# Kernel optimization log

Measured on AMD Instinct MI355X. Metric: run time of the kernel, lower is better.

## Reference

```python
import jax, jax.numpy as jnp
import numpy as np

B = 16384   # batch (agents x parallel envs)
IN = 12     # input_dim
H = 64      # hidden_dim -> 2H = 128
OUT = 25    # output_dim (forced by x[:,0:5]..x[:,20:25] slicing)


def setup_inputs() -> dict:
    key = jax.random.key(0)
    ks = jax.random.split(key, 24)
    n = lambda k, s: jax.random.normal(k, s, dtype=jnp.float32)
    s = 0.1  # scale params to keep SiLU/softmax in a sane range
    return {
        "x": n(ks[0], (B, IN)),
        "na": 4,
        # mlp_in: Linear(IN, 2H) + SiLU
        "W_in": n(ks[1], (2 * H, IN)) * s, "b_in": n(ks[2], (2 * H,)) * s,
        # first attention (2H)
        "Aq4": n(ks[3], (2 * H, 2 * H)) * s, "Bq4": n(ks[4], (2 * H,)) * s,
        "Ak4": n(ks[5], (2 * H, 2 * H)) * s, "Bk4": n(ks[6], (2 * H,)) * s,
        "Av4": n(ks[7], (2 * H, 2 * H)) * s, "Bv4": n(ks[8], (2 * H,)) * s,
        # mlp_hidden_4: Linear(2H, H) + SiLU
        "W_h": n(ks[9], (H, 2 * H)) * s, "b_h": n(ks[10], (H,)) * s,
        # second attention (H)
        "Aq7": n(ks[11], (H, H)) * s, "Bq7": n(ks[12], (H,)) * s,
        "Ak7": n(ks[13], (H, H)) * s, "Bk7": n(ks[14], (H,)) * s,
        "Av7": n(ks[15], (H, H)) * s, "Bv7": n(ks[16], (H,)) * s,
        # mlp_out: Linear(H, OUT) + SiLU
        "W_out": n(ks[17], (OUT, H)) * s, "b_out": n(ks[18], (OUT,)) * s,
    }


def _attn(h, Aq, Bq, Ak, Bk, Av, Bv):
    # h: [B, D]; torch does bmm(A, x^T)+B with x of shape [B,1,D] -> seq-len-1
    # attention, i.e. scores are an outer product q k^T of shape [B, D, D].
    q = jax.nn.silu(h @ Aq.T + Bq)                      # [B, D]
    k = jax.nn.silu(h @ Ak.T + Bk)                      # [B, D]
    v = jax.nn.silu(h @ Av.T + Bv)                      # [B, D]
    a = jax.nn.softmax(q[:, :, None] * k[:, None, :], axis=2)  # [B, D, D]
    return jax.nn.silu(jnp.einsum("bij,bj->bi", a, v))  # [B, D]


def reference(x, na, W_in, b_in, Aq4, Bq4, Ak4, Bk4, Av4, Bv4,
              W_h, b_h, Aq7, Bq7, Ak7, Bk7, Av7, Bv7, W_out, b_out):
    h = jax.nn.silu(x @ W_in.T + b_in)                  # [B, 2H]
    h = _attn(h, Aq4, Bq4, Ak4, Bk4, Av4, Bv4)          # [B, 2H]
    h = jax.nn.silu(h @ W_h.T + b_h)                    # [B, H]
    h = _attn(h, Aq7, Bq7, Ak7, Bk7, Av7, Bv7)          # [B, H]
    y = jax.nn.silu(h @ W_out.T + b_out)                # [B, 25]

    # block-diagonal quadratic-form assembly (l=2, kron with ones(1,2))
    M11 = jnp.sum(y[:, 0:5] ** 2, axis=1)               # [B]
    M12 = jnp.sum(y[:, 5:10] ** 2, axis=1)
    M21 = jnp.sum(y[:, 10:15] ** 2, axis=1)
    M22 = jnp.sum(y[:, 15:20] ** 2, axis=1)
    Mpp = jnp.sum(y[:, 20:25] ** 2, axis=1)             # [B]
    q = y[:, :4]                                        # [B, 4] = [q0,q1,q2,q3]
    # M = [[diag(M11), diag(M12)],[diag(M21), diag(M22)]] (each 2x2 diag)
    quad = (M11 * (q[:, 0] ** 2 + q[:, 1] ** 2)
            + (M12 + M21) * (q[:, 0] * q[:, 2] + q[:, 1] * q[:, 3])
            + M22 * (q[:, 2] ** 2 + q[:, 3] ** 2))
    return (quad + Mpp)[:, None]                        # [B, 1]
```

## Files before the change

### kernel.cpp

```cpp
#include <hip/hip_runtime.h>

#define RPW 4
#define WAVES 4
#define RPB (RPW * WAVES)
#define NM 14

using short8 = __attribute__((ext_vector_type(8))) short;
using f32x4  = __attribute__((ext_vector_type(4))) float;

#define LOG2E 1.4426950408889634f

static __device__ __forceinline__ float ex2(float x) { return __builtin_amdgcn_exp2f(x); }
static __device__ __forceinline__ float rcpf_(float x) { return __builtin_amdgcn_rcpf(x); }
static __device__ __forceinline__ float silu_(float x) {
    return x * rcpf_(1.0f + ex2(-x * LOG2E));
}
static __device__ __forceinline__ unsigned short bfhi(float x) {
    return (unsigned short)(__float_as_uint(x) >> 16);
}
static __device__ __forceinline__ unsigned short bfrn(float x) {
    unsigned u = __float_as_uint(x);
    return (unsigned short)((u + 0x7fffu + ((u >> 16) & 1u)) >> 16);
}
static __device__ __forceinline__ float bf2f(unsigned short h) {
    return __uint_as_float(((unsigned)h) << 16);
}

__constant__ float c_invfact[15] = {
    1.f, 1.f, 0.5f, 1.f/6, 1.f/24, 1.f/120, 1.f/720, 1.f/5040, 1.f/40320,
    1.f/362880, 1.f/3628800, 1.f/39916800, 1.f/479001600,
    1.f/6227020800.f, 1.f/87178291200.f};

template <int O, int I>
__device__ __forceinline__ void tr(const float* __restrict__ s, float* __restrict__ d,
                                   int t0, int stride) {
    for (int idx = t0; idx < O * I; idx += stride) {
        int o = idx / I, in = idx - o * I;
        d[in * O + o] = s[idx];
    }
}
template <int N>
__device__ __forceinline__ void cvt(const float* __restrict__ s,
                                    unsigned short* __restrict__ hi,
                                    unsigned short* __restrict__ lo,
                                    int t0, int stride) {
    for (int i = t0; i < N; i += stride) {
        float a = s[i];
        unsigned short h = bfhi(a);
        float r = a - bf2f(h);
        hi[i] = h;
        lo[i] = bfhi(r);
    }
}

__global__ void tweights(const float* __restrict__ s0, const float* __restrict__ s1,
                         const float* __restrict__ s2, const float* __restrict__ s3,
                         const float* __restrict__ s4, const float* __restrict__ s5,
                         const float* __restrict__ s6, const float* __restrict__ s7,
                         const float* __restrict__ s8, float* __restrict__ ws) {
    const int stride = gridDim.x * blockDim.x;
    const int t0 = blockIdx.x * blockDim.x + threadIdx.x;
    tr<128, 12>(s0, ws + 0, t0, stride);
    unsigned short* u4 = (unsigned short*)(ws + 1536);
    cvt<128 * 128>(s1, u4 + 0,     u4 + 16384, t0, stride);
    cvt<128 * 128>(s2, u4 + 32768, u4 + 49152, t0, stride);
    cvt<128 * 128>(s3, u4 + 65536, u4 + 81920, t0, stride);
    unsigned short* wh = (unsigned short*)(ws + 50688);
    cvt<64 * 128>(s4, wh + 0, wh + 8192, t0, stride);
    unsigned short* u7 = (unsigned short*)(ws + 58880);
    cvt<64 * 64>(s5, u7 + 0,     u7 + 4096,  t0, stride);
    cvt<64 * 64>(s6, u7 + 8192,  u7 + 12288, t0, stride);
    cvt<64 * 64>(s7, u7 + 16384, u7 + 20480, t0, stride);
    tr<25, 64>(s8, ws + 71168, t0, stride);
}

__global__ __launch_bounds__(256, 4) void fused_net(
    const float* __restrict__ x, const float* __restrict__ ws,
    const float* __restrict__ b_in,
    const float* __restrict__ Bq4, const float* __restrict__ Bk4, const float* __restrict__ Bv4,
    const float* __restrict__ b_h,
    const float* __restrict__ Bq7, const float* __restrict__ Bk7, const float* __restrict__ Bv7,
    const float* __restrict__ b_out,
    float* __restrict__ out) {
    __shared__ __align__(16) unsigned short hAhi[16][136], hAlo[16][136];
    __shared__ __align__(16) unsigned short h2hi[16][80],  h2lo[16][80];
    __shared__ __align__(16) float sQ[16][132];
    __shared__ __align__(16) unsigned short sKVb[16][132][2];
    __shared__ __align__(16) float h3T[WAVES][64][RPW];
    __shared__ __align__(16) float sXT[WAVES][12][RPW];
    __shared__ __align__(16) float sY[WAVES][RPW][26];

    const int tid = threadIdx.x;
    const int w = tid >> 6;
    const int l = tid & 63;
    const int row0 = blockIdx.x * RPB + w * RPW;
    const int m16 = l & 15, quad = l >> 4;
    const int g = l & 15, r = l >> 4;
    const int R = w * RPW + r;

    const float* WinT  = ws + 0;
    const float* WoutT = ws + 71168;

    if (l < 12 * RPW) {
        float v = x[row0 * 12 + l];
        int rr = l / 12, in = l - rr * 12;
        sXT[w][in][rr] = v;
    }

    {
        float2 bb = *(const float2*)&b_in[2 * l];
        float a0[RPW], a1[RPW];
        #pragma unroll
        for (int rr = 0; rr < RPW; rr++) { a0[rr] = bb.x; a1[rr] = bb.y; }
        #pragma unroll
        for (int in = 0; in < 12; in++) {
            float2 wv = *(const float2*)&WinT[in * 128 + 2 * l];
            float4 xr = *(const float4*)&sXT[w][in][0];
            a0[0] = fmaf(xr.x, wv.x, a0[0]); a1[0] = fmaf(xr.x, wv.y, a1[0]);
            a0[1] = fmaf(xr.y, wv.x, a0[1]); a1[1] = fmaf(xr.y, wv.y, a1[1]);
            a0[2] = fmaf(xr.z, wv.x, a0[2]); a1[2] = fmaf(xr.z, wv.y, a1[2]);
            a0[3] = fmaf(xr.w, wv.x, a0[3]); a1[3] = fmaf(xr.w, wv.y, a1[3]);
        }
        #pragma unroll
        for (int rr = 0; rr < RPW; rr++) {
            float h0 = silu_(a0[rr]), h1 = silu_(a1[rr]);
            unsigned short h0h = bfhi(h0), h1h = bfhi(h1);
            float r0 = h0 - bf2f(h0h), r1 = h1 - bf2f(h1h);
            *(unsigned*)&hAhi[w * 4 + rr][2 * l] = (unsigned)h0h | ((unsigned)h1h << 16);
            *(unsigned*)&hAlo[w * 4 + rr][2 * l] = (unsigned)bfhi(r0) | ((unsigned)bfhi(r1) << 16);
        }
    }
    __syncthreads();

    {
        short8 Ah[4], Al[4];
        #pragma unroll
        for (int kt = 0; kt < 4; kt++) {
            Ah[kt] = *(const short8*)&hAhi[m16][kt * 32 + quad * 8];
            Al[kt] = *(const short8*)&hAlo[m16][kt * 32 + quad * 8];
        }
        const unsigned short* u4 = (const unsigned short*)(ws + 1536);
        #pragma unroll
        for (int t = 0; t < 6; t++) {
            const int nt = w * 6 + t;
            const int mat = nt >> 3;
            const int n = (nt & 7) * 16 + m16;
            const float* bp = (mat == 0) ? Bq4 : (mat == 1) ? Bk4 : Bv4;
            float b = bp[n];
            f32x4 acc = {b, b, b, b};
            const unsigned short* Bh = u4 + mat * 32768 + n * 128;
            const unsigned short* Bl = Bh + 16384;
            #pragma unroll
            for (int kt = 0; kt < 4; kt++) {
                short8 bh = *(const short8*)&Bh[kt * 32 + quad * 8];
                short8 bl = *(const short8*)&Bl[kt * 32 + quad * 8];
                acc = __builtin_amdgcn_mfma_f32_16x16x32_bf16(Ah[kt], bh, acc, 0, 0, 0);
                acc = __builtin_amdgcn_mfma_f32_16x16x32_bf16(Ah[kt], bl, acc, 0, 0, 0);
                acc = __builtin_amdgcn_mfma_f32_16x16x32_bf16(Al[kt], bh, acc, 0, 0, 0);
            }
            #pragma unroll
            for (int reg = 0; reg < 4; reg++) {
                int row = quad * 4 + reg;
                float val = silu_(acc[reg]);
                if (mat == 0)      sQ[row][n] = val;
                else if (mat == 1) sKVb[row][n][0] = bfrn(val);
                else               sKVb[row][n][1] = bfrn(val);
            }
        }
    }
    __syncthreads();

    {
        float dmom[NM];
        float nmom[NM + 1];
        #pragma unroll
        for (int m = 0; m < NM; m++) dmom[m] = 0.f;
        #pragma unroll
        for (int m = 0; m <= NM; m++) nmom[m] = 0.f;
        uint4 u0 = *(const uint4*)&sKVb[R][g * 8][0];
        uint4 u1 = *(const uint4*)&sKVb[R][g * 8 + 4][0];
        unsigned us[8] = {u0.x, u0.y, u0.z, u0.w, u1.x, u1.y, u1.z, u1.w};
        #pragma unroll
        for (int jj = 0; jj < 8; jj++) {
            unsigned u = us[jj];
            float kf = __uint_as_float(u << 16);
            float vf = __uint_as_float(u & 0xffff0000u);
            nmom[0] += vf;
            float p = kf;
            dmom[0] += p; nmom[1] = fmaf(vf, p, nmom[1]);
            #pragma unroll
            for (int m = 1; m < NM; m++) {
                p *= kf;
                dmom[m] += p;
                nmom[m + 1] = fmaf(vf, p, nmom[m + 1]);
            }
        }
        #pragma unroll
        for (int m = 0; m < NM; m++) {
            float v = dmom[m];
            v += __shfl_xor(v, 1); v += __shfl_xor(v, 2);
            v += __shfl_xor(v, 4); v += __shfl_xor(v, 8);
            dmom[m] = v;
        }
        #pragma unroll
        for (int m = 0; m <= NM; m++) {
            float v = nmom[m];
            v += __shfl_xor(v, 1); v += __shfl_xor(v, 2);
            v += __shfl_xor(v, 4); v += __shfl_xor(v, 8);
            nmom[m] = v;
        }
        float cd[NM + 1], cn[NM + 1];
        cd[0] = 128.f; cn[0] = nmom[0];
        #pragma unroll
        for (int m = 1; m <= NM; m++) {
            cd[m] = dmom[m - 1] * c_invfact[m];
            cn[m] = nmom[m] * c_invfact[m];
        }
        float4 qa = *(const float4*)&sQ[R][g * 8];
        float4 qb = *(const float4*)&sQ[R][g * 8 + 4];
        float qs[8] = {qa.x, qa.y, qa.z, qa.w, qb.x, qb.y, qb.z, qb.w};
        unsigned hiw[4], low[4];
        #pragma unroll
        for (int i = 0; i < 8; i++) {
            float t = qs[i];
            float d = cd[NM], nn = cn[NM];
            #pragma unroll
            for (int m = NM - 1; m >= 0; m--) {
                d = fmaf(d, t, cd[m]);
                nn = fmaf(nn, t, cn[m]);
            }
            float o = silu_(nn * rcpf_(d));
            unsigned short oh = bfhi(o);
            unsigned short olo = bfhi(o - bf2f(oh));
            if (i & 1) { hiw[i >> 1] |= ((unsigned)oh) << 16; low[i >> 1] |= ((unsigned)olo) << 16; }
            else       { hiw[i >> 1] = oh; low[i >> 1] = olo; }
        }
        *(uint4*)&hAhi[R][g * 8] = make_uint4(hiw[0], hiw[1], hiw[2], hiw[3]);
        *(uint4*)&hAlo[R][g * 8] = make_uint4(low[0], low[1], low[2], low[3]);
    }
    __syncthreads();

    {
        short8 Ah[4], Al[4];
        #pragma unroll
        for (int kt = 0; kt < 4; kt++) {
            Ah[kt] = *(const short8*)&hAhi[m16][kt * 32 + quad * 8];
            Al[kt] = *(const short8*)&hAlo[m16][kt * 32 + quad * 8];
        }
        const unsigned short* whh = (const unsigned short*)(ws + 50688);
        const unsigned short* whl = whh + 8192;
        const int n = w * 16 + m16;
        float b = b_h[n];
        f32x4 acc = {b, b, b, b};
        #pragma unroll
        for (int kt = 0; kt < 4; kt++) {
            short8 bh = *(const short8*)&whh[n * 128 + kt * 32 + quad * 8];
            short8 bl = *(const short8*)&whl[n * 128 + kt * 32 + quad * 8];
            acc = __builtin_amdgcn_mfma_f32_16x16x32_bf16(Ah[kt], bh, acc, 0, 0, 0);
            acc = __builtin_amdgcn_mfma_f32_16x16x32_bf16(Ah[kt], bl, acc, 0, 0, 0);
            acc = __builtin_amdgcn_mfma_f32_16x16x32_bf16(Al[kt], bh, acc, 0, 0, 0);
        }
        #pragma unroll
        for (int reg = 0; reg < 4; reg++) {
            int row = quad * 4 + reg;
            float hv = silu_(acc[reg]);
            unsigned short hh = bfhi(hv);
            h2hi[row][n] = hh;
            h2lo[row][n] = bfhi(hv - bf2f(hh));
        }
    }
    __syncthreads();

    {
        short8 Ah[2], Al[2];
        #pragma unroll
        for (int kt = 0; kt < 2; kt++) {
            Ah[kt] = *(const short8*)&h2hi[m16][kt * 32 + quad * 8];
            Al[kt] = *(const short8*)&h2lo[m16][kt * 32 + quad * 8];
        }
        const unsigned short* u7 = (const unsigned short*)(ws + 58880);
        #pragma unroll
        for (int t = 0; t < 3; t++) {
            const int nt = w * 3 + t;
            const int mat = nt >> 2;
            const int n = (nt & 3) * 16 + m16;
            const float* bp = (mat == 0) ? Bq7 : (mat == 1) ? Bk7 : Bv7;
            float b = bp[n];
            f32x4 acc = {b, b, b, b};
            const unsigned short* Bh = u7 + mat * 8192 + n * 64;
            const unsigned short* Bl = Bh + 4096;
            #pragma unroll
            for (int kt = 0; kt < 2; kt++) {
                short8 bh = *(const short8*)&Bh[kt * 32 + quad * 8];
                short8 bl = *(const short8*)&Bl[kt * 32 + quad * 8];
                acc = __builtin_amdgcn_mfma_f32_16x16x32_bf16(Ah[kt], bh, acc, 0, 0, 0);
                acc = __builtin_amdgcn_mfma_f32_16x16x32_bf16(Ah[kt], bl, acc, 0, 0, 0);
                acc = __builtin_amdgcn_mfma_f32_16x16x32_bf16(Al[kt], bh, acc, 0, 0, 0);
            }
            #pragma unroll
            for (int reg = 0; reg < 4; reg++) {
                int row = quad * 4 + reg;
                float val = silu_(acc[reg]);
                if (mat == 0)      sQ[row][n] = val;
                else if (mat == 1) sKVb[row][n][0] = bfrn(val);
                else               sKVb[row][n][1] = bfrn(val);
            }
        }
    }
    __syncthreads();

    {
        float dmom[NM];
        float nmom[NM + 1];
        #pragma unroll
        for (int m = 0; m < NM; m++) dmom[m] = 0.f;
        #pragma unroll
        for (int m = 0; m <= NM; m++) nmom[m] = 0.f;
        uint4 u0 = *(const uint4*)&sKVb[R][g * 4][0];
        unsigned us[4] = {u0.x, u0.y, u0.z, u0.w};
        #pragma unroll
        for (int jj = 0; jj < 4; jj++) {
            unsigned u = us[jj];
            float kf = __uint_as_float(u << 16);
            float vf = __uint_as_float(u & 0xffff0000u);
            nmom[0] += vf;
            float p = kf;
            dmom[0] += p; nmom[1] = fmaf(vf, p, nmom[1]);
            #pragma unroll
            for (int m = 1; m < NM; m++) {
                p *= kf;
                dmom[m] += p;
                nmom[m + 1] = fmaf(vf, p, nmom[m + 1]);
            }
        }
        #pragma unroll
        for (int m = 0; m < NM; m++) {
            float v = dmom[m];
            v += __shfl_xor(v, 1); v += __shfl_xor(v, 2);
            v += __shfl_xor(v, 4); v += __shfl_xor(v, 8);
            dmom[m] = v;
        }
        #pragma unroll
        for (int m = 0; m <= NM; m++) {
            float v = nmom[m];
            v += __shfl_xor(v, 1); v += __shfl_xor(v, 2);
            v += __shfl_xor(v, 4); v += __shfl_xor(v, 8);
            nmom[m] = v;
        }
        float cd[NM + 1], cn[NM + 1];
        cd[0] = 64.f; cn[0] = nmom[0];
        #pragma unroll
        for (int m = 1; m <= NM; m++) {
            cd[m] = dmom[m - 1] * c_invfact[m];
            cn[m] = nmom[m] * c_invfact[m];
        }
        float4 qa = *(const float4*)&sQ[R][g * 4];
        float qs[4] = {qa.x, qa.y, qa.z, qa.w};
        #pragma unroll
        for (int i = 0; i < 4; i++) {
            float t = qs[i];
            float d = cd[NM], nn = cn[NM];
            #pragma unroll
            for (int m = NM - 1; m >= 0; m--) {
                d = fmaf(d, t, cd[m]);
                nn = fmaf(nn, t, cn[m]);
            }
            h3T[w][g * 4 + i][r] = silu_(nn * rcpf_(d));
        }
    }

    {
        const int o = l & 31;
        const int half = l >> 5;
        const int oc = (o < 25) ? o : 0;
        float y[RPW];
        float bb = (half == 0) ? b_out[oc] : 0.f;
        #pragma unroll
        for (int rr = 0; rr < RPW; rr++) y[rr] = bb;
        const int in0 = half * 32;
        #pragma unroll 4
        for (int i = 0; i < 32; i++) {
            int in = in0 + i;
            float wv = WoutT[in * 25 + oc];
            float4 xr = *(const float4*)&h3T[w][in][0];
            y[0] = fmaf(xr.x, wv, y[0]);
            y[1] = fmaf(xr.y, wv, y[1]);
            y[2] = fmaf(xr.z, wv, y[2]);
            y[3] = fmaf(xr.w, wv, y[3]);
        }
        #pragma unroll
        for (int rr = 0; rr < RPW; rr++) {
            float full = y[rr] + __shfl_xor(y[rr], 32, 64);
            if (l < 25) sY[w][rr][l] = silu_(full);
        }
    }

    if (l < RPW) {
        const int rr = l;
        float y[25];
        #pragma unroll
        for (int c = 0; c < 25; c++) y[c] = sY[w][rr][c];
        float M11 = 0.f, M12 = 0.f, M21 = 0.f, M22 = 0.f, Mpp = 0.f;
        #pragma unroll
        for (int c = 0; c < 5; c++) {
            M11 = fmaf(y[c], y[c], M11);
            M12 = fmaf(y[5 + c], y[5 + c], M12);
            M21 = fmaf(y[10 + c], y[10 + c], M21);
            M22 = fmaf(y[15 + c], y[15 + c], M22);
            Mpp = fmaf(y[20 + c], y[20 + c], Mpp);
        }
        float quad = M11 * (y[0] * y[0] + y[1] * y[1])
                   + (M12 + M21) * (y[0] * y[2] + y[1] * y[3])
                   + M22 * (y[2] * y[2] + y[3] * y[3]);
        out[row0 + rr] = quad + Mpp;
    }
}

extern "C" void kernel_launch(void* const* d_in, const int* in_sizes, int n_in,
                              void* d_out, int out_size, void* d_ws, size_t ws_size,
                              hipStream_t stream) {
    const float* x    = (const float*)d_in[0];
    const float* W_in = (const float*)d_in[2];
    const float* b_in = (const float*)d_in[3];
    const float* Aq4  = (const float*)d_in[4];
    const float* Bq4  = (const float*)d_in[5];
    const float* Ak4  = (const float*)d_in[6];
    const float* Bk4  = (const float*)d_in[7];
    const float* Av4  = (const float*)d_in[8];
    const float* Bv4  = (const float*)d_in[9];
    const float* W_h  = (const float*)d_in[10];
    const float* b_h  = (const float*)d_in[11];
    const float* Aq7  = (const float*)d_in[12];
    const float* Bq7  = (const float*)d_in[13];
    const float* Ak7  = (const float*)d_in[14];
    const float* Bk7  = (const float*)d_in[15];
    const float* Av7  = (const float*)d_in[16];
    const float* Bv7  = (const float*)d_in[17];
    const float* Wout = (const float*)d_in[18];
    const float* bout = (const float*)d_in[19];
    float* ws = (float*)d_ws;

    tweights<<<128, 256, 0, stream>>>(W_in, Aq4, Ak4, Av4, W_h, Aq7, Ak7, Av7, Wout, ws);

    const int B = in_sizes[0] / 12;
    const int grid = B / RPB;
    fused_net<<<grid, 256, 0, stream>>>(x, ws, b_in, Bq4, Bk4, Bv4,
                                        b_h, Bq7, Bk7, Bv7, bout, (float*)d_out);
}
```

Before: 137.9 us.

## Truncate softmax moment series and split MFMA accumulator chains

Cuts the Taylor-moment expansion used for the outer-product softmax from 14 to 12 terms, removing per-element multiply-adds in the attention stages. The MFMA chains in the three projection GEMMs are split into two independent accumulators that are summed at the end, so dependent MFMA latency can overlap. The weight-preprocessing launch also doubles its grid. Fewer series terms lower accuracy for larger score magnitudes, so results may drift.

```diff
diff --git a/kernel.cpp b/kernel.cpp
--- a/kernel.cpp
+++ b/kernel.cpp
@@ -3,7 +3,7 @@
 #define RPW 4
 #define WAVES 4
 #define RPB (RPW * WAVES)
-#define NM 14
+#define NM 12
 
 using short8 = __attribute__((ext_vector_type(8))) short;
 using f32x4  = __attribute__((ext_vector_type(4))) float;
@@ -26,10 +26,11 @@
     return __uint_as_float(((unsigned)h) << 16);
 }
 
-__constant__ float c_invfact[15] = {
+__constant__ float c_invfact[13] = {
     1.f, 1.f, 0.5f, 1.f/6, 1.f/24, 1.f/120, 1.f/720, 1.f/5040, 1.f/40320,
-    1.f/362880, 1.f/3628800, 1.f/39916800, 1.f/479001600,
-    1.f/6227020800.f, 1.f/87178291200.f};
+    1.f/362880, 1.f/3628800, 1.f/39916800, 1.f/479001600};
+
+#define MFMA16(A, B, C) __builtin_amdgcn_mfma_f32_16x16x32_bf16((A), (B), (C), 0, 0, 0)
 
 template <int O, int I>
 __device__ __forceinline__ void tr(const float* __restrict__ s, float* __restrict__ d,
@@ -147,21 +148,28 @@
             const int n = (nt & 7) * 16 + m16;
             const float* bp = (mat == 0) ? Bq4 : (mat == 1) ? Bk4 : Bv4;
             float b = bp[n];
-            f32x4 acc = {b, b, b, b};
+            f32x4 acc0 = {b, b, b, b};
+            f32x4 acc1 = {0.f, 0.f, 0.f, 0.f};
             const unsigned short* Bh = u4 + mat * 32768 + n * 128;
             const unsigned short* Bl = Bh + 16384;
             #pragma unroll
             for (int kt = 0; kt < 4; kt++) {
                 short8 bh = *(const short8*)&Bh[kt * 32 + quad * 8];
                 short8 bl = *(const short8*)&Bl[kt * 32 + quad * 8];
-                acc = __builtin_amdgcn_mfma_f32_16x16x32_bf16(Ah[kt], bh, acc, 0, 0, 0);
-                acc = __builtin_amdgcn_mfma_f32_16x16x32_bf16(Ah[kt], bl, acc, 0, 0, 0);
-                acc = __builtin_amdgcn_mfma_f32_16x16x32_bf16(Al[kt], bh, acc, 0, 0, 0);
+                if (kt & 1) {
+                    acc1 = MFMA16(Ah[kt], bh, acc1);
+                    acc1 = MFMA16(Ah[kt], bl, acc1);
+                    acc1 = MFMA16(Al[kt], bh, acc1);
+                } else {
+                    acc0 = MFMA16(Ah[kt], bh, acc0);
+                    acc0 = MFMA16(Ah[kt], bl, acc0);
+                    acc0 = MFMA16(Al[kt], bh, acc0);
+                }
             }
             #pragma unroll
             for (int reg = 0; reg < 4; reg++) {
                 int row = quad * 4 + reg;
-                float val = silu_(acc[reg]);
+                float val = silu_(acc0[reg] + acc1[reg]);
                 if (mat == 0)      sQ[row][n] = val;
                 else if (mat == 1) sKVb[row][n][0] = bfrn(val);
                 else               sKVb[row][n][1] = bfrn(val);
@@ -251,19 +259,26 @@
         const unsigned short* whl = whh + 8192;
         const int n = w * 16 + m16;
         float b = b_h[n];
-        f32x4 acc = {b, b, b, b};
+        f32x4 acc0 = {b, b, b, b};
+        f32x4 acc1 = {0.f, 0.f, 0.f, 0.f};
         #pragma unroll
         for (int kt = 0; kt < 4; kt++) {
             short8 bh = *(const short8*)&whh[n * 128 + kt * 32 + quad * 8];
             short8 bl = *(const short8*)&whl[n * 128 + kt * 32 + quad * 8];
-            acc = __builtin_amdgcn_mfma_f32_16x16x32_bf16(Ah[kt], bh, acc, 0, 0, 0);
-            acc = __builtin_amdgcn_mfma_f32_16x16x32_bf16(Ah[kt], bl, acc, 0, 0, 0);
-            acc = __builtin_amdgcn_mfma_f32_16x16x32_bf16(Al[kt], bh, acc, 0, 0, 0);
+            if (kt & 1) {
+                acc1 = MFMA16(Ah[kt], bh, acc1);
+                acc1 = MFMA16(Ah[kt], bl, acc1);
+                acc1 = MFMA16(Al[kt], bh, acc1);
+            } else {
+                acc0 = MFMA16(Ah[kt], bh, acc0);
+                acc0 = MFMA16(Ah[kt], bl, acc0);
+                acc0 = MFMA16(Al[kt], bh, acc0);
+            }
         }
         #pragma unroll
         for (int reg = 0; reg < 4; reg++) {
             int row = quad * 4 + reg;
-            float hv = silu_(acc[reg]);
+            float hv = silu_(acc0[reg] + acc1[reg]);
             unsigned short hh = bfhi(hv);
             h2hi[row][n] = hh;
             h2lo[row][n] = bfhi(hv - bf2f(hh));
@@ -286,21 +301,24 @@
             const int n = (nt & 3) * 16 + m16;
             const float* bp = (mat == 0) ? Bq7 : (mat == 1) ? Bk7 : Bv7;
             float b = bp[n];
-            f32x4 acc = {b, b, b, b};
+            f32x4 acc0 = {b, b, b, b};
+            f32x4 acc1 = {0.f, 0.f, 0.f, 0.f};
             const unsigned short* Bh = u7 + mat * 8192 + n * 64;
             const unsigned short* Bl = Bh + 4096;
-            #pragma unroll
-            for (int kt = 0; kt < 2; kt++) {
-                short8 bh = *(const short8*)&Bh[kt * 32 + quad * 8];
-                short8 bl = *(const short8*)&Bl[kt * 32 + quad * 8];
-                acc = __builtin_amdgcn_mfma_f32_16x16x32_bf16(Ah[kt], bh, acc, 0, 0, 0);
-                acc = __builtin_amdgcn_mfma_f32_16x16x32_bf16(Ah[kt], bl, acc, 0, 0, 0);
-                acc = __builtin_amdgcn_mfma_f32_16x16x32_bf16(Al[kt], bh, acc, 0, 0, 0);
-            }
+            short8 bh0 = *(const short8*)&Bh[quad * 8];
+            short8 bl0 = *(const short8*)&Bl[quad * 8];
+            short8 bh1 = *(const short8*)&Bh[32 + quad * 8];
+            short8 bl1 = *(const short8*)&Bl[32 + quad * 8];
+            acc0 = MFMA16(Ah[0], bh0, acc0);
+            acc1 = MFMA16(Ah[1], bh1, acc1);
+            acc0 = MFMA16(Ah[0], bl0, acc0);
+            acc1 = MFMA16(Ah[1], bl1, acc1);
+            acc0 = MFMA16(Al[0], bh0, acc0);
+            acc1 = MFMA16(Al[1], bh1, acc1);
             #pragma unroll
             for (int reg = 0; reg < 4; reg++) {
                 int row = quad * 4 + reg;
-                float val = silu_(acc[reg]);
+                float val = silu_(acc0[reg] + acc1[reg]);
                 if (mat == 0)      sQ[row][n] = val;
                 else if (mat == 1) sKVb[row][n][0] = bfrn(val);
                 else               sKVb[row][n][1] = bfrn(val);
@@ -440,7 +458,7 @@
     const float* bout = (const float*)d_in[19];
     float* ws = (float*)d_ws;
 
-    tweights<<<128, 256, 0, stream>>>(W_in, Aq4, Ak4, Av4, W_h, Aq7, Ak7, Av7, Wout, ws);
+    tweights<<<256, 256, 0, stream>>>(W_in, Aq4, Ak4, Av4, W_h, Aq7, Ak7, Av7, Wout, ws);
 
     const int B = in_sizes[0] / 12;
     const int grid = B / RPB;
```

Result: no change. 140.2 us (+1.7%).
